# Kernel optimization log

Measured on AMD Instinct MI355X. Metric: run time of the kernel, lower is better.

Reference implementation:

```python
import jax, jax.numpy as jnp
import numpy as np

C = 1.5          # Poincare ball curvature (geoopt PoincareBallExact(c=1.5))
TEMP = 0.1       # logits temperature
EPS = 1e-5       # artanh clamp, matches geoopt fp32 eps


def _mlp(x, w1, b1, w2, b2, w3, b3):
    # torch nn.GELU default is the exact erf formulation
    h = jax.nn.gelu(x @ w1 + b1, approximate=False)
    h = jax.nn.gelu(h @ w2 + b2, approximate=False)
    return h @ w3 + b3


def _expmap0(u):
    # geoopt expmap0: tanh(sqrt(c)*||u||) * u / (sqrt(c)*||u||)
    sqrt_c = jnp.sqrt(C)
    n = jnp.maximum(jnp.linalg.norm(u, axis=-1, keepdims=True), 1e-15)
    return jnp.tanh(sqrt_c * n) * u / (sqrt_c * n)


def _poincare_dist(protos, y):
    """Pairwise Poincare distance. protos: (P, d) on-ball, y: (B, d) on-ball -> (B, P).
    dist(x, y) = 2/sqrt(c) * artanh(sqrt(c) * ||mobius_add(-x, y)||)
    """
    sqrt_c = jnp.sqrt(C)
    x = -protos                               # (P, d)
    x2 = jnp.sum(x * x, axis=-1)              # (P,)
    y2 = jnp.sum(y * y, axis=-1)              # (B,)
    xy = y @ x.T                              # (B, P) = <x, y> broadcast
    a = 1.0 + 2.0 * C * xy + C * y2[:, None]  # coeff of x
    b = 1.0 - C * x2[None, :]                 # coeff of y
    denom = 1.0 + 2.0 * C * xy + (C * C) * x2[None, :] * y2[:, None]
    denom = jnp.maximum(jnp.abs(denom), 1e-15)
    # only one (B, P, d) intermediate: the mobius-add numerator
    num = a[:, :, None] * x[None, :, :] + b[:, :, None] * y[:, None, :]
    r = sqrt_c * jnp.linalg.norm(num, axis=-1) / denom   # (B, P)
    r = jnp.clip(r, 0.0, 1.0 - EPS)
    return (2.0 / sqrt_c) * jnp.arctanh(r)


def setup_inputs() -> dict:
    key = jax.random.key(0)
    ks = jax.random.split(key, 16)
    B, DIN, H, D = 64, 768, 4096, 256
    PG, PS = 500, 5000

    def lin(kw, kb, fan_in, fan_out):
        s = 1.0 / np.sqrt(fan_in)
        w = jax.random.uniform(kw, (fan_in, fan_out), jnp.float32, -s, s)
        b = jax.random.uniform(kb, (fan_out,), jnp.float32, -s, s)
        return w, b

    x = jax.random.normal(ks[0], (B, DIN), jnp.float32)
    # prototypes: random points well inside the ball (radius 1/sqrt(1.5) ~ 0.816)
    protos_genus = 0.01 * jax.random.normal(ks[1], (PG, D), jnp.float32)
    protos_species = 0.01 * jax.random.normal(ks[2], (PS, D), jnp.float32)

    w1g, b1g = lin(ks[3], ks[4], DIN, H)
    w2g, b2g = lin(ks[5], ks[6], H, H)
    w3g, b3g = lin(ks[7], ks[8], H, D)
    w1s, b1s = lin(ks[9], ks[10], DIN, H)
    w2s, b2s = lin(ks[11], ks[12], H, H)
    w3s, b3s = lin(ks[13], ks[14], H, D)

    return {
        "x": x, "protos_genus": protos_genus, "protos_species": protos_species,
        "w1g": w1g, "b1g": b1g, "w2g": w2g, "b2g": b2g, "w3g": w3g, "b3g": b3g,
        "w1s": w1s, "b1s": b1s, "w2s": w2s, "b2s": b2s, "w3s": w3s, "b3s": b3s,
    }


def reference(x, protos_genus, protos_species,
              w1g, b1g, w2g, b2g, w3g, b3g,
              w1s, b1s, w2s, b2s, w3s, b3s):
    feat_g = _mlp(x, w1g, b1g, w2g, b2g, w3g, b3g)   # (B, D) euclidean
    feat_s = _mlp(x, w1s, b1s, w2s, b2s, w3s, b3s)
    hyp_g = _expmap0(feat_g)
    hyp_s = _expmap0(feat_s)
    logits_g = -_poincare_dist(protos_genus, hyp_g) / TEMP    # (B, PG)
    logits_s = -_poincare_dist(protos_species, hyp_s) / TEMP  # (B, PS)
    return (logits_g, logits_s)
```

## Files before the change

kernel.cpp:

```cpp
#include <hip/hip_runtime.h>
#include <hip/hip_bf16.h>
#include <math.h>

typedef unsigned short ushort_t;
typedef unsigned int uint_t;

#define C_CURV 1.5f
#define SQRT_C 1.22474487139158905f
#define TEMP_ 0.1f

typedef __attribute__((ext_vector_type(8))) short short8;
typedef __attribute__((ext_vector_type(4))) float f32x4;

static __device__ __forceinline__ ushort_t f2bf(float f) {
  union { float f; uint_t u; } v; v.f = f;
  uint_t u = v.u;
  uint_t r = (u + 0x7FFFu + ((u >> 16) & 1u)) >> 16;
  return (ushort_t)r;
}

static __device__ __forceinline__ float b2f(ushort_t h) {
  union { uint_t u; float f; } v; v.u = ((uint_t)h) << 16;
  return v.f;
}

static __device__ __forceinline__ float gelu_exact(float x) {
  return 0.5f * x * (1.0f + erff(x * 0.70710678118654752f));
}

__global__ void k_cvt_x(const float* __restrict__ x, ushort_t* __restrict__ xb, int n4) {
  int i = blockIdx.x * blockDim.x + threadIdx.x;
  if (i >= n4) return;
  float4 v = reinterpret_cast<const float4*>(x)[i];
  ushort4 o;
  o.x = f2bf(v.x); o.y = f2bf(v.y); o.z = f2bf(v.z); o.w = f2bf(v.w);
  reinterpret_cast<ushort4*>(xb)[i] = o;
}

__global__ __launch_bounds__(512, 4) void k_gemm(
    const ushort_t* __restrict__ Abase, long a_br_stride,
    const float* __restrict__ Wg, const float* __restrict__ Ws,
    ushort_t* __restrict__ partial, int N, int K, int kchunk)
{
  __shared__ float    sW[2][32][128];
  __shared__ ushort_t sA[2][64][32];

  const int tn = blockIdx.x, ks = blockIdx.y, br = blockIdx.z;
  const int KS = gridDim.y;
  const ushort_t* A = Abase + (long)br * a_br_stride;
  const float* W = br ? Ws : Wg;
  const int lane = threadIdx.x & 63;
  const int w = threadIdx.x >> 6;
  const int c = lane & 15;
  const int g = lane >> 4;
  const int n0b = tn * 128;
  const int k0 = ks * kchunk;
  const bool hasA = (w < 4);

  const float* wst = W + (long)(k0 + w * 4 + (lane >> 5)) * N + n0b + (lane & 31) * 4;
  const ushort_t* ast = A + (long)(w * 16 + (lane >> 2)) * K + k0 + (lane & 3) * 8;

  f32x4 acc[4];
  #pragma unroll
  for (int mi = 0; mi < 4; ++mi) acc[mi] = f32x4{0.f, 0.f, 0.f, 0.f};

  float4 w0A, w1A; uint4 aA;
  float4 w0B, w1B; uint4 aB;

#define LOADREG(S, T) do { \
    w0##S = *reinterpret_cast<const float4*>(wst + (long)((T) * 32) * N); \
    w1##S = *reinterpret_cast<const float4*>(wst + (long)((T) * 32 + 2) * N); \
    if (hasA) a##S = *reinterpret_cast<const uint4*>(ast + (T) * 32); \
  } while (0)

#define DSWRITE(S, B) do { \
    *reinterpret_cast<float4*>(&sW[B][w * 4 + (lane >> 5)][(lane & 31) * 4]) = w0##S; \
    *reinterpret_cast<float4*>(&sW[B][w * 4 + 2 + (lane >> 5)][(lane & 31) * 4]) = w1##S; \
    if (hasA) *reinterpret_cast<uint4*>(&sA[B][w * 16 + (lane >> 2)][(lane & 3) * 8]) = a##S; \
  } while (0)

#define COMPUTE(B) do { \
    short8 af[4]; \
    _Pragma("unroll") for (int mi = 0; mi < 4; ++mi) \
      af[mi] = *reinterpret_cast<const short8*>(&sA[B][c + 16 * mi][8 * g]); \
    float bw[8]; \
    _Pragma("unroll") for (int j = 0; j < 8; ++j) \
      bw[j] = sW[B][8 * g + j][w * 16 + c]; \
    short8 bf; \
    _Pragma("unroll") for (int j = 0; j < 8; ++j) bf[j] = (short)f2bf(bw[j]); \
    _Pragma("unroll") for (int mi = 0; mi < 4; ++mi) \
      acc[mi] = __builtin_amdgcn_mfma_f32_16x16x32_bf16(af[mi], bf, acc[mi], 0, 0, 0); \
  } while (0)

#define ITER(CUR, NXT, T) do { \
    if ((T) + 1 < nt) LOADREG(NXT, (T) + 1); \
    __builtin_amdgcn_sched_barrier(0); \
    DSWRITE(CUR, (T) & 1); \
    asm volatile("s_waitcnt lgkmcnt(0)" ::: "memory"); \
    __builtin_amdgcn_sched_barrier(0); \
    __builtin_amdgcn_s_barrier(); \
    __builtin_amdgcn_sched_barrier(0); \
    COMPUTE((T) & 1); \
  } while (0)

  const int nt = kchunk >> 5;
  LOADREG(A, 0);
  int t = 0;
  for (; t + 1 < nt; t += 2) {
    ITER(A, B, t);
    ITER(B, A, t + 1);
  }
  if (nt & 1) ITER(A, B, nt - 1);
#undef LOADREG
#undef DSWRITE
#undef COMPUTE
#undef ITER

  ushort_t* po = partial + (long)(br * KS + ks) * 64 * N;
  const int n0 = n0b + w * 16 + c;
  #pragma unroll
  for (int mi = 0; mi < 4; ++mi)
    #pragma unroll
    for (int q = 0; q < 4; ++q) {
      int b = 16 * mi + 4 * g + q;
      po[(long)b * N + n0] = f2bf(acc[mi][q]);
    }
}

__global__ void k_reduce_gelu(const ushort_t* __restrict__ partial,
    const float* __restrict__ bg, const float* __restrict__ bs,
    ushort_t* __restrict__ hb, int N, int KS, int total8)
{
  int i = blockIdx.x * blockDim.x + threadIdx.x;
  if (i >= total8) return;
  int perbr8 = 64 * N / 8;
  int br = i / perbr8;
  int rem = i - br * perbr8;
  const short8* pp = reinterpret_cast<const short8*>(partial) + (long)br * KS * perbr8 + rem;
  float s[8] = {0.f, 0.f, 0.f, 0.f, 0.f, 0.f, 0.f, 0.f};
  for (int ks = 0; ks < KS; ++ks) {
    short8 t = pp[(long)ks * perbr8];
    #pragma unroll
    for (int j = 0; j < 8; ++j) s[j] += b2f((ushort_t)t[j]);
  }
  int n8 = rem % (N / 8);
  float4 bv0 = reinterpret_cast<const float4*>(br ? bs : bg)[n8 * 2];
  float4 bv1 = reinterpret_cast<const float4*>(br ? bs : bg)[n8 * 2 + 1];
  s[0] += bv0.x; s[1] += bv0.y; s[2] += bv0.z; s[3] += bv0.w;
  s[4] += bv1.x; s[5] += bv1.y; s[6] += bv1.z; s[7] += bv1.w;
  short8 o;
  #pragma unroll
  for (int j = 0; j < 8; ++j) o[j] = (short)f2bf(gelu_exact(s[j]));
  reinterpret_cast<short8*>(hb)[i] = o;
}

__global__ __launch_bounds__(256) void k_expmap(const ushort_t* __restrict__ partial,
    const float* __restrict__ b3g, const float* __restrict__ b3s,
    ushort_t* __restrict__ hypb, float* __restrict__ y2, int KS)
{
  int b = blockIdx.x, br = blockIdx.y, d = threadIdx.x;
  const ushort_t* pp = partial + (long)(br * KS) * 64 * 256 + (long)b * 256 + d;
  float s = 0.f;
  #pragma unroll 8
  for (int ks = 0; ks < KS; ++ks) s += b2f(pp[(long)ks * 64 * 256]);
  s += (br ? b3s : b3g)[d];

  float v = s * s;
  #pragma unroll
  for (int off = 1; off < 64; off <<= 1) v += __shfl_xor(v, off);
  __shared__ float red[4];
  __shared__ float n2s;
  if ((threadIdx.x & 63) == 0) red[threadIdx.x >> 6] = v;
  __syncthreads();
  if (threadIdx.x == 0) n2s = red[0] + red[1] + red[2] + red[3];
  __syncthreads();
  float n = fmaxf(sqrtf(n2s), 1e-15f);
  float sn = SQRT_C * n;
  float t = tanhf(sn);
  float scale = t / sn;
  hypb[((long)br * 64 + b) * 256 + d] = f2bf(s * scale);
  if (threadIdx.x == 0) y2[br * 64 + b] = t * t / C_CURV;
}

__global__ __launch_bounds__(256) void k_dist(const float* __restrict__ pg,
    const float* __restrict__ ps, const ushort_t* __restrict__ hypb,
    const float* __restrict__ y2, float* __restrict__ out)
{
  int u = blockIdx.x * 4 + (threadIdx.x >> 6);
  const int lane = threadIdx.x & 63;
  const int c = lane & 15, g = lane >> 4;
  const float* protos; const ushort_t* A; const float* y2p; float* ob; int P;
  if (u < 128) {
    protos = pg; P = 500; A = hypb; y2p = y2; ob = out;
  } else {
    u -= 128;
    if (u >= 1252) return;
    protos = ps; P = 5000; A = hypb + 64 * 256; y2p = y2 + 64; ob = out + 64 * 500;
  }
  const int w = u >> 2;
  const int mi = u & 3;
  int p = w * 16 + c;
  int pc = min(p, P - 1);
  const float* pp = protos + (long)pc * 256 + 8 * g;
  const ushort_t* ap = A + (long)(c + 16 * mi) * 256 + 8 * g;

  f32x4 acc = {0.f, 0.f, 0.f, 0.f};
  float x2p = 0.f;

  #pragma unroll
  for (int s8 = 0; s8 < 8; ++s8) {
    float4 v0 = *reinterpret_cast<const float4*>(pp + 32 * s8);
    float4 v1 = *reinterpret_cast<const float4*>(pp + 32 * s8 + 4);
    x2p += v0.x * v0.x + v0.y * v0.y + v0.z * v0.z + v0.w * v0.w
         + v1.x * v1.x + v1.y * v1.y + v1.z * v1.z + v1.w * v1.w;
    short8 bfr;
    bfr[0] = (short)f2bf(v0.x); bfr[1] = (short)f2bf(v0.y);
    bfr[2] = (short)f2bf(v0.z); bfr[3] = (short)f2bf(v0.w);
    bfr[4] = (short)f2bf(v1.x); bfr[5] = (short)f2bf(v1.y);
    bfr[6] = (short)f2bf(v1.z); bfr[7] = (short)f2bf(v1.w);
    short8 af = *reinterpret_cast<const short8*>(ap + 32 * s8);
    acc = __builtin_amdgcn_mfma_f32_16x16x32_bf16(af, bfr, acc, 0, 0, 0);
  }
  x2p += __shfl_xor(x2p, 16);
  x2p += __shfl_xor(x2p, 32);
  const float x2 = x2p;
  const float bb = 1.f - C_CURV * x2;
  const float LC = -2.f / (SQRT_C * TEMP_);

  if (p < P) {
    #pragma unroll
    for (int q = 0; q < 4; ++q) {
      int b = 16 * mi + 4 * g + q;
      float xy = -acc[q];
      float y2v = y2p[b];
      float a = 1.f + 2.f * C_CURV * xy + C_CURV * y2v;
      float den = fabsf(1.f + 2.f * C_CURV * xy + C_CURV * C_CURV * x2 * y2v);
      den = fmaxf(den, 1e-15f);
      float num2 = a * a * x2 + 2.f * a * bb * xy + bb * bb * y2v;
      num2 = fmaxf(num2, 0.f);
      float r = SQRT_C * sqrtf(num2) / den;
      r = fminf(r, 1.f - 1e-5f);
      r = fmaxf(r, 0.f);
      ob[(long)b * P + p] = LC * atanhf(r);
    }
  }
}

extern "C" void kernel_launch(void* const* d_in, const int* in_sizes, int n_in,
                              void* d_out, int out_size, void* d_ws, size_t ws_size,
                              hipStream_t stream) {
  const float* x   = (const float*)d_in[0];
  const float* pg  = (const float*)d_in[1];
  const float* ps  = (const float*)d_in[2];
  const float* w1g = (const float*)d_in[3];
  const float* b1g = (const float*)d_in[4];
  const float* w2g = (const float*)d_in[5];
  const float* b2g = (const float*)d_in[6];
  const float* w3g = (const float*)d_in[7];
  const float* b3g = (const float*)d_in[8];
  const float* w1s = (const float*)d_in[9];
  const float* b1s = (const float*)d_in[10];
  const float* w2s = (const float*)d_in[11];
  const float* b2s = (const float*)d_in[12];
  const float* w3s = (const float*)d_in[13];
  const float* b3s = (const float*)d_in[14];
  float* out = (float*)d_out;
  char* ws = (char*)d_ws;
  (void)in_sizes; (void)n_in; (void)out_size; (void)ws_size;

  const int KS1 = 8, KS2 = 16, KS3 = 64;
  size_t PART = (size_t)KS2 * 2 * 64 * 4096 * 2;

  ushort_t* partial = (ushort_t*)(ws);
  ushort_t* xb      = (ushort_t*)(ws + PART);
  ushort_t* h1b     = (ushort_t*)(ws + PART + 98304);
  ushort_t* h2b     = (ushort_t*)(ws + PART + 98304 + 1048576);
  ushort_t* hypb    = (ushort_t*)(ws + PART + 98304 + 2097152);
  float*    y2      = (float*)   (ws + PART + 98304 + 2097152 + 65536);

  k_cvt_x<<<48, 256, 0, stream>>>(x, xb, 64 * 768 / 4);
  k_gemm<<<dim3(32, KS1, 2), 512, 0, stream>>>(xb, 0L, w1g, w1s, partial, 4096, 768, 768 / KS1);
  k_reduce_gelu<<<256, 256, 0, stream>>>(partial, b1g, b1s, h1b, 4096, KS1, 2 * 64 * 4096 / 8);
  k_gemm<<<dim3(32, KS2, 2), 512, 0, stream>>>(h1b, (long)64 * 4096, w2g, w2s, partial, 4096, 4096, 4096 / KS2);
  k_reduce_gelu<<<256, 256, 0, stream>>>(partial, b2g, b2s, h2b, 4096, KS2, 2 * 64 * 4096 / 8);
  k_gemm<<<dim3(2, KS3, 2), 512, 0, stream>>>(h2b, (long)64 * 4096, w3g, w3s, partial, 256, 4096, 4096 / KS3);
  k_expmap<<<dim3(64, 2), 256, 0, stream>>>(partial, b3g, b3s, hypb, y2, KS3);
  k_dist<<<345, 256, 0, stream>>>(pg, ps, hypb, y2, out);
}
```

Baseline: 78.01 us.

## Double K-tile depth, prefetch two tiles ahead, and reduce split-K factors

The GEMM kernel now stages 64-wide K tiles instead of 32, with all 512 threads loading both A and W. Register prefetch is deepened to three rotating buffers so global loads run two tiles ahead of compute. Split-K factors drop (8→6, 16→8, 64→32), which means fewer partial sums to write and reduce but fewer blocks in flight. Shared memory doubles to about 80KB per block, which may limit occupancy, and each thread holds more prefetch registers.

```diff
diff --git a/kernel.cpp b/kernel.cpp
--- a/kernel.cpp
+++ b/kernel.cpp
@@ -42,58 +42,68 @@
     const float* __restrict__ Wg, const float* __restrict__ Ws,
     ushort_t* __restrict__ partial, int N, int K, int kchunk)
 {
-  __shared__ float    sW[2][32][128];
-  __shared__ ushort_t sA[2][64][32];
+  __shared__ float    sW[2][64][128];
+  __shared__ ushort_t sA[2][64][64];
 
   const int tn = blockIdx.x, ks = blockIdx.y, br = blockIdx.z;
   const int KS = gridDim.y;
   const ushort_t* A = Abase + (long)br * a_br_stride;
   const float* W = br ? Ws : Wg;
-  const int lane = threadIdx.x & 63;
-  const int w = threadIdx.x >> 6;
+  const int tid = threadIdx.x;
+  const int lane = tid & 63;
+  const int w = tid >> 6;
   const int c = lane & 15;
   const int g = lane >> 4;
   const int n0b = tn * 128;
   const int k0 = ks * kchunk;
-  const bool hasA = (w < 4);
-
-  const float* wst = W + (long)(k0 + w * 4 + (lane >> 5)) * N + n0b + (lane & 31) * 4;
-  const ushort_t* ast = A + (long)(w * 16 + (lane >> 2)) * K + k0 + (lane & 3) * 8;
+
+  const int srow = tid >> 3;
+  const int wcol = (tid & 7) * 16;
+  const int akoff = (tid & 7) * 8;
+
+  const float* wst = W + (long)(k0 + srow) * N + n0b + wcol;
+  const ushort_t* ast = A + (long)srow * K + k0 + akoff;
 
   f32x4 acc[4];
   #pragma unroll
   for (int mi = 0; mi < 4; ++mi) acc[mi] = f32x4{0.f, 0.f, 0.f, 0.f};
 
-  float4 w0A, w1A; uint4 aA;
-  float4 w0B, w1B; uint4 aB;
+  float4 wvA0, wvA1, wvA2, wvA3; uint4 avA;
+  float4 wvB0, wvB1, wvB2, wvB3; uint4 avB;
+  float4 wvC0, wvC1, wvC2, wvC3; uint4 avC;
 
 #define LOADREG(S, T) do { \
-    w0##S = *reinterpret_cast<const float4*>(wst + (long)((T) * 32) * N); \
-    w1##S = *reinterpret_cast<const float4*>(wst + (long)((T) * 32 + 2) * N); \
-    if (hasA) a##S = *reinterpret_cast<const uint4*>(ast + (T) * 32); \
+    const float* wp_ = wst + (long)((T) * 64) * N; \
+    wv##S##0 = *reinterpret_cast<const float4*>(wp_); \
+    wv##S##1 = *reinterpret_cast<const float4*>(wp_ + 4); \
+    wv##S##2 = *reinterpret_cast<const float4*>(wp_ + 8); \
+    wv##S##3 = *reinterpret_cast<const float4*>(wp_ + 12); \
+    av##S = *reinterpret_cast<const uint4*>(ast + (T) * 64); \
   } while (0)
 
 #define DSWRITE(S, B) do { \
-    *reinterpret_cast<float4*>(&sW[B][w * 4 + (lane >> 5)][(lane & 31) * 4]) = w0##S; \
-    *reinterpret_cast<float4*>(&sW[B][w * 4 + 2 + (lane >> 5)][(lane & 31) * 4]) = w1##S; \
-    if (hasA) *reinterpret_cast<uint4*>(&sA[B][w * 16 + (lane >> 2)][(lane & 3) * 8]) = a##S; \
+    float4* wd_ = reinterpret_cast<float4*>(&sW[B][srow][wcol]); \
+    wd_[0] = wv##S##0; wd_[1] = wv##S##1; wd_[2] = wv##S##2; wd_[3] = wv##S##3; \
+    *reinterpret_cast<uint4*>(&sA[B][srow][akoff]) = av##S; \
   } while (0)
 
 #define COMPUTE(B) do { \
-    short8 af[4]; \
-    _Pragma("unroll") for (int mi = 0; mi < 4; ++mi) \
-      af[mi] = *reinterpret_cast<const short8*>(&sA[B][c + 16 * mi][8 * g]); \
-    float bw[8]; \
-    _Pragma("unroll") for (int j = 0; j < 8; ++j) \
-      bw[j] = sW[B][8 * g + j][w * 16 + c]; \
-    short8 bf; \
-    _Pragma("unroll") for (int j = 0; j < 8; ++j) bf[j] = (short)f2bf(bw[j]); \
-    _Pragma("unroll") for (int mi = 0; mi < 4; ++mi) \
-      acc[mi] = __builtin_amdgcn_mfma_f32_16x16x32_bf16(af[mi], bf, acc[mi], 0, 0, 0); \
-  } while (0)
-
-#define ITER(CUR, NXT, T) do { \
-    if ((T) + 1 < nt) LOADREG(NXT, (T) + 1); \
+    _Pragma("unroll") for (int kk = 0; kk < 64; kk += 32) { \
+      short8 af[4]; \
+      _Pragma("unroll") for (int mi = 0; mi < 4; ++mi) \
+        af[mi] = *reinterpret_cast<const short8*>(&sA[B][c + 16 * mi][kk + 8 * g]); \
+      float bw[8]; \
+      _Pragma("unroll") for (int j = 0; j < 8; ++j) \
+        bw[j] = sW[B][kk + 8 * g + j][w * 16 + c]; \
+      short8 bf; \
+      _Pragma("unroll") for (int j = 0; j < 8; ++j) bf[j] = (short)f2bf(bw[j]); \
+      _Pragma("unroll") for (int mi = 0; mi < 4; ++mi) \
+        acc[mi] = __builtin_amdgcn_mfma_f32_16x16x32_bf16(af[mi], bf, acc[mi], 0, 0, 0); \
+    } \
+  } while (0)
+
+#define ITER(CUR, NXT2, T) do { \
+    if ((T) + 2 < nt) LOADREG(NXT2, (T) + 2); \
     __builtin_amdgcn_sched_barrier(0); \
     DSWRITE(CUR, (T) & 1); \
     asm volatile("s_waitcnt lgkmcnt(0)" ::: "memory"); \
@@ -103,14 +113,14 @@
     COMPUTE((T) & 1); \
   } while (0)
 
-  const int nt = kchunk >> 5;
+  const int nt = kchunk >> 6;
   LOADREG(A, 0);
-  int t = 0;
-  for (; t + 1 < nt; t += 2) {
-    ITER(A, B, t);
-    ITER(B, A, t + 1);
-  }
-  if (nt & 1) ITER(A, B, nt - 1);
+  if (nt > 1) LOADREG(B, 1);
+  for (int t = 0; t < nt; t += 3) {
+    ITER(A, C, t);
+    if (t + 1 < nt) ITER(B, A, t + 1);
+    if (t + 2 < nt) ITER(C, B, t + 2);
+  }
 #undef LOADREG
 #undef DSWRITE
 #undef COMPUTE
@@ -268,7 +278,7 @@
   char* ws = (char*)d_ws;
   (void)in_sizes; (void)n_in; (void)out_size; (void)ws_size;
 
-  const int KS1 = 8, KS2 = 16, KS3 = 64;
+  const int KS1 = 6, KS2 = 8, KS3 = 32;
   size_t PART = (size_t)KS2 * 2 * 64 * 4096 * 2;
 
   ushort_t* partial = (ushort_t*)(ws);
```

New measurement: 77.67 us. About the same (-0.4%).
